# Kernel optimization log

Hardware: AMD Instinct MI355X
Metric: run time of the kernel (lower is better)

The kernel has to match this reference:

```python
import jax, jax.numpy as jnp
import numpy as np

NUM_HEADS = 8


def _attention(q, k, v, num_heads):
    # q,k,v: [L/S, N, E] seq-first (torch MHA convention)
    L, N, E = q.shape
    S = k.shape[0]
    hd = E // num_heads
    qh = q.reshape(L, N, num_heads, hd).transpose(1, 2, 0, 3)  # [N,H,L,hd]
    kh = k.reshape(S, N, num_heads, hd).transpose(1, 2, 0, 3)  # [N,H,S,hd]
    vh = v.reshape(S, N, num_heads, hd).transpose(1, 2, 0, 3)  # [N,H,S,hd]
    scale = 1.0 / np.sqrt(hd).astype(np.float32)
    scores = jnp.einsum('bhld,bhsd->bhls', qh * scale, kh)  # [N,H,L,S]
    probs = jax.nn.softmax(scores, axis=-1)
    out = jnp.einsum('bhls,bhsd->bhld', probs, vh)  # [N,H,L,hd]
    return out.transpose(2, 0, 1, 3).reshape(L, N, E)


def setup_inputs() -> dict:
    key = jax.random.key(0)
    ks = jax.random.split(key, 20)
    L, N, E = 1024, 8, 256
    s = 1.0 / np.sqrt(E)
    inp = {}
    names = ['query', 'key', 'value', 'query_teacher', 'key_teacher', 'value_teacher']
    for i, n in enumerate(names):
        inp[n] = jax.random.normal(ks[i], (L, N, E), dtype=jnp.float32)
    wnames = ['w_q', 'w_k', 'w_v', 'w_q_teacher', 'w_k_teacher', 'w_v_teacher', 'w_out', 'w_out_teacher']
    for i, n in enumerate(wnames):
        inp[n] = jax.random.normal(ks[6 + i], (E, E), dtype=jnp.float32) * s
    for n in ['b_q', 'b_k', 'b_v', 'b_q_teacher', 'b_k_teacher', 'b_v_teacher', 'b_out', 'b_out_teacher']:
        inp[n] = jnp.zeros((E,), dtype=jnp.float32)
    return inp


def reference(query, key, value, query_teacher, key_teacher, value_teacher,
              w_q, w_k, w_v, b_q, b_k, b_v,
              w_q_teacher, w_k_teacher, w_v_teacher, b_q_teacher, b_k_teacher, b_v_teacher,
              w_out, b_out, w_out_teacher, b_out_teacher):
    # Six separate in-projections (student + teacher), torch linear: x @ W.T + b
    Q = query @ w_q.T + b_q
    K = key @ w_k.T + b_k
    V = value @ w_v.T + b_v
    Qt = query_teacher @ w_q_teacher.T + b_q_teacher
    Kt = key_teacher @ w_k_teacher.T + b_k_teacher
    Vt = value_teacher @ w_v_teacher.T + b_v_teacher
    # Two attention streams
    out_s = _attention(Q, K, V, NUM_HEADS)
    out_t = _attention(Qt, Kt, Vt, NUM_HEADS)
    # Separate out-projections
    out_s = out_s @ w_out.T + b_out
    out_t = out_t @ w_out_teacher.T + b_out_teacher
    return out_s, out_t
```

## Files before the change

kernel.cpp:

```cpp
#include <hip/hip_runtime.h>

typedef __attribute__((ext_vector_type(4))) float f32x4;
typedef __attribute__((ext_vector_type(16))) float f32x16;
typedef __attribute__((ext_vector_type(8))) __bf16 bf16x8;
typedef __attribute__((ext_vector_type(4))) __bf16 bf16x4;

#define L_SEQ 1024
#define NB 8
#define EMB 256
#define NHEAD 8
#define HD 32
#define MROWS 8192
#define SZ_ELEM ((size_t)MROWS * EMB)

static __device__ __forceinline__ f32x4 mfma_bf16(bf16x8 a, bf16x8 b, f32x4 c) {
    return __builtin_amdgcn_mfma_f32_16x16x32_bf16(a, b, c, 0, 0, 0);
}
static __device__ __forceinline__ f32x16 mfma32(bf16x8 a, bf16x8 b, f32x16 c) {
    return __builtin_amdgcn_mfma_f32_32x32x16_bf16(a, b, c, 0, 0, 0);
}

static __device__ __forceinline__ unsigned pack2(float a, float b) {
    union { __bf16 h; unsigned short u; } lo, hi;
    lo.h = (__bf16)a; hi.h = (__bf16)b;
    return (unsigned)lo.u | ((unsigned)hi.u << 16);
}

static __device__ __forceinline__ void permswap(unsigned &a, unsigned &b) {
    asm("v_permlane32_swap_b32 %0, %1" : "+v"(a), "+v"(b));
}

struct GemmBatch {
    const void* X[6];
    const float* W[6];
    const float* Bv[6];
    void* O[6];
    float scale[6];
};

template<int XMODE, bool OUT_F32>
__global__ __launch_bounds__(256, 2)
void gemm_kernel(GemmBatch batch) {
    __shared__ __bf16 Xl[128][72];
    __shared__ __bf16 Wl[64][72];
    const int z = blockIdx.z;
    const int fid = blockIdx.x;
    const int swz = (fid & 7) * 32 + (fid >> 3);
    const int nblk = swz & 3, mblk = swz >> 2;
    const float* __restrict__ W = batch.W[z];
    const float* __restrict__ bias = batch.Bv[z];
    const float scale = batch.scale[z];
    const int tid = threadIdx.x;
    const int w = tid >> 6, lane = tid & 63;
    const int g = lane >> 4, li = lane & 15;
    const int wr = w >> 1, wc = w & 1;

    f32x4 acc[4][2];
#pragma unroll
    for (int i = 0; i < 4; ++i)
#pragma unroll
        for (int j = 0; j < 2; ++j) acc[i][j] = f32x4{0.f, 0.f, 0.f, 0.f};

    for (int kk = 0; kk < 4; ++kk) {
        __syncthreads();
        if (XMODE == 1) {
            const __bf16* Xb = (const __bf16*)batch.X[z];
#pragma unroll
            for (int p = 0; p < 4; ++p) {
                int idx = tid + p * 256;
                int row = idx >> 3, c8 = (idx & 7) * 8;
                bf16x8 xv = *(const bf16x8*)(Xb + (size_t)(mblk * 128 + row) * 256 + kk * 64 + c8);
                *(bf16x8*)&Xl[row][c8] = xv;
            }
        } else {
            const float* Xf = (const float*)batch.X[z];
#pragma unroll
            for (int p = 0; p < 8; ++p) {
                int idx = tid + p * 256;
                int row = idx >> 4, c4 = (idx & 15) * 4;
                f32x4 xv = *(const f32x4*)(Xf + (size_t)(mblk * 128 + row) * 256 + kk * 64 + c4);
                bf16x4 bv;
#pragma unroll
                for (int j = 0; j < 4; ++j) bv[j] = (__bf16)xv[j];
                *(bf16x4*)&Xl[row][c4] = bv;
            }
        }
#pragma unroll
        for (int p = 0; p < 4; ++p) {
            int idx = tid + p * 256;
            int row = idx >> 4, c4 = (idx & 15) * 4;
            f32x4 wv = *(const f32x4*)(W + (size_t)(nblk * 64 + row) * 256 + kk * 64 + c4);
            bf16x4 bv;
#pragma unroll
            for (int j = 0; j < 4; ++j) bv[j] = (__bf16)wv[j];
            *(bf16x4*)&Wl[row][c4] = bv;
        }
        __syncthreads();
#pragma unroll
        for (int ks = 0; ks < 2; ++ks) {
            bf16x8 a[4], b[2];
#pragma unroll
            for (int af = 0; af < 4; ++af)
                a[af] = *(const bf16x8*)&Xl[wr * 64 + af * 16 + li][ks * 32 + g * 8];
#pragma unroll
            for (int bi = 0; bi < 2; ++bi)
                b[bi] = *(const bf16x8*)&Wl[wc * 32 + bi * 16 + li][ks * 32 + g * 8];
#pragma unroll
            for (int af = 0; af < 4; ++af)
#pragma unroll
                for (int bi = 0; bi < 2; ++bi)
                    acc[af][bi] = mfma_bf16(a[af], b[bi], acc[af][bi]);
        }
    }
#pragma unroll
    for (int af = 0; af < 4; ++af)
#pragma unroll
        for (int bi = 0; bi < 2; ++bi)
#pragma unroll
            for (int r = 0; r < 4; ++r) {
                int mrow = mblk * 128 + wr * 64 + af * 16 + 4 * g + r;
                int ncol = nblk * 64 + wc * 32 + bi * 16 + li;
                float v = (acc[af][bi][r] + bias[ncol]) * scale;
                if (OUT_F32)
                    ((float*)batch.O[z])[(size_t)mrow * 256 + ncol] = v;
                else
                    ((__bf16*)batch.O[z])[(size_t)mrow * 256 + ncol] = (__bf16)v;
            }
}

struct AttnArgs {
    const __bf16* Q[2];
    const __bf16* K[2];
    const __bf16* V[2];
    __bf16* AO[2];
};

__global__ __launch_bounds__(256, 4)
void attn_kernel(AttnArgs args) {
    __shared__ __bf16 Kl[128][40];
    __shared__ __bf16 Vt[32][136];
    const int fid = blockIdx.x;
    const int swz = (fid & 7) * 128 + (fid >> 3);
    const int qb = swz & 7;
    const int nh = (swz >> 3) & 63;
    const int st = swz >> 9;
    const int n = nh >> 3, h = nh & 7;
    const __bf16* __restrict__ Q = args.Q[st];
    const __bf16* __restrict__ K = args.K[st];
    const __bf16* __restrict__ V = args.V[st];
    __bf16* __restrict__ AO = args.AO[st];
    const int tid = threadIdx.x;
    const int w = tid >> 6, lane = tid & 63;
    const int q32 = lane & 31, hi = lane >> 5;

    bf16x8 qf[2];
    {
        int qrow = qb * 128 + w * 32 + q32;
#pragma unroll
        for (int kb = 0; kb < 2; ++kb)
            qf[kb] = *(const bf16x8*)(Q + ((size_t)qrow * NB + n) * EMB + h * HD + kb * 16 + hi * 8);
    }

    bf16x8 ones;
#pragma unroll
    for (int j = 0; j < 8; ++j) ones[j] = (__bf16)1.0f;

    f32x16 accO, accL;
#pragma unroll
    for (int r = 0; r < 16; ++r) { accO[r] = 0.f; accL[r] = 0.f; }

    const int vsw_r = ((q32 >> 3) & 3) << 3;

    for (int t = 0; t < 8; ++t) {
        const int s0 = t * 128;
        __syncthreads();
#pragma unroll
        for (int p = 0; p < 2; ++p) {
            int idx = tid + p * 256;
            int row = idx >> 2, c8 = (idx & 3) * 8;
            size_t gaddr = ((size_t)(s0 + row) * NB + n) * EMB + h * HD + c8;
            *(bf16x8*)&Kl[row][c8] = *(const bf16x8*)(K + gaddr);
            bf16x8 vv = *(const bf16x8*)(V + gaddr);
#pragma unroll
            for (int j = 0; j < 8; ++j) {
                int d = c8 + j;
                Vt[d][row ^ (((d >> 3) & 3) << 3)] = vv[j];
            }
        }
        __syncthreads();

#pragma unroll
        for (int sb = 0; sb < 4; ++sb) {
            bf16x8 kf0 = *(const bf16x8*)&Kl[sb * 32 + q32][hi * 8];
            bf16x8 kf1 = *(const bf16x8*)&Kl[sb * 32 + q32][16 + hi * 8];
            f32x16 s;
#pragma unroll
            for (int r = 0; r < 16; ++r) s[r] = -12.0f;
            __builtin_amdgcn_s_setprio(1);
            s = mfma32(kf0, qf[0], s);
            s = mfma32(kf1, qf[1], s);
            __builtin_amdgcn_s_setprio(0);
            float p[16];
#pragma unroll
            for (int r = 0; r < 16; ++r) p[r] = __builtin_amdgcn_exp2f(s[r]);

            bf16x8 pa[2];
#pragma unroll
            for (int ks = 0; ks < 2; ++ks) {
                unsigned x0 = pack2(p[8 * ks + 0], p[8 * ks + 1]);
                unsigned x1 = pack2(p[8 * ks + 2], p[8 * ks + 3]);
                unsigned x2 = pack2(p[8 * ks + 4], p[8 * ks + 5]);
                unsigned x3 = pack2(p[8 * ks + 6], p[8 * ks + 7]);
                permswap(x0, x2);
                permswap(x1, x3);
                union { unsigned u[4]; bf16x8 v; } cvt;
                cvt.u[0] = x0; cvt.u[1] = x1; cvt.u[2] = x2; cvt.u[3] = x3;
                pa[ks] = cvt.v;
            }
            bf16x8 vf0 = *(const bf16x8*)&Vt[q32][(sb * 32 + hi * 8) ^ vsw_r];
            bf16x8 vf1 = *(const bf16x8*)&Vt[q32][(sb * 32 + 16 + hi * 8) ^ vsw_r];
            __builtin_amdgcn_s_setprio(1);
            accO = mfma32(pa[0], vf0, accO);
            accL = mfma32(pa[0], ones, accL);
            accO = mfma32(pa[1], vf1, accO);
            accL = mfma32(pa[1], ones, accL);
            __builtin_amdgcn_s_setprio(0);
        }
    }

#pragma unroll
    for (int r = 0; r < 16; ++r) {
        int crow = (r & 3) + 8 * (r >> 2) + 4 * hi;
        int row = qb * 128 + w * 32 + crow;
        AO[((size_t)row * NB + n) * EMB + h * HD + q32] = (__bf16)(accO[r] / accL[r]);
    }
}

extern "C" void kernel_launch(void* const* d_in, const int* in_sizes, int n_in,
                              void* d_out, int out_size, void* d_ws, size_t ws_size,
                              hipStream_t stream) {
    const size_t SZ = SZ_ELEM;
    __bf16* wsb = (__bf16*)d_ws;
    __bf16* arr[8];
    for (int i = 0; i < 8; ++i) arr[i] = wsb + (size_t)i * SZ;

    const float qscale = 0.25504310349362475f;

    GemmBatch pb{};
    for (int s = 0; s < 6; ++s) {
        pb.X[s] = d_in[s];
        pb.W[s] = (const float*)d_in[6 + s];
        pb.Bv[s] = (const float*)d_in[14 + s];
        pb.O[s] = arr[s];
        pb.scale[s] = (s == 0 || s == 3) ? qscale : 1.0f;
    }
    hipLaunchKernelGGL((gemm_kernel<0, false>), dim3(256, 1, 6), dim3(256), 0, stream, pb);

    AttnArgs aa{};
    aa.Q[0] = arr[0]; aa.K[0] = arr[1]; aa.V[0] = arr[2]; aa.AO[0] = arr[6];
    aa.Q[1] = arr[3]; aa.K[1] = arr[4]; aa.V[1] = arr[5]; aa.AO[1] = arr[7];
    hipLaunchKernelGGL(attn_kernel, dim3(1024), dim3(256), 0, stream, aa);

    GemmBatch ob{};
    for (int s = 0; s < 2; ++s) {
        ob.X[s] = arr[6 + s];
        ob.W[s] = (const float*)d_in[12 + s];
        ob.Bv[s] = (const float*)d_in[20 + s];
        ob.O[s] = (float*)d_out + (size_t)s * SZ;
        ob.scale[s] = 1.0f;
    }
    hipLaunchKernelGGL((gemm_kernel<1, true>), dim3(256, 1, 2), dim3(256), 0, stream, ob);
}
```

Before: 73.81 us.

## Double-buffer K/V shared tiles with register prefetch in attention loop

Attention now prefetches the next 128-row K/V tile into registers at the start of each iteration and writes it into a second LDS buffer after the compute phase. The goal is to hide global-load latency behind the QK/PV MFMA work. In exchange it doubles the LDS footprint and adds prefetch registers, which can lower occupancy. The score accumulator initialisation is also hoisted into a constant vector.

```diff
diff --git a/kernel.cpp b/kernel.cpp
--- a/kernel.cpp
+++ b/kernel.cpp
@@ -137,8 +137,8 @@
 
 __global__ __launch_bounds__(256, 4)
 void attn_kernel(AttnArgs args) {
-    __shared__ __bf16 Kl[128][40];
-    __shared__ __bf16 Vt[32][136];
+    __shared__ __bf16 Kl[2][128][40];
+    __shared__ __bf16 Vt[2][32][136];
     const int fid = blockIdx.x;
     const int swz = (fid & 7) * 128 + (fid >> 3);
     const int qb = swz & 7;
@@ -164,6 +164,9 @@
     bf16x8 ones;
 #pragma unroll
     for (int j = 0; j < 8; ++j) ones[j] = (__bf16)1.0f;
+    f32x16 minit;
+#pragma unroll
+    for (int r = 0; r < 16; ++r) minit[r] = -12.0f;
 
     f32x16 accO, accL;
 #pragma unroll
@@ -171,33 +174,41 @@
 
     const int vsw_r = ((q32 >> 3) & 3) << 3;
 
+    const int srow0 = tid >> 2, c8s = (tid & 3) * 8;
+    const int srow1 = srow0 + 64;
+
+    bf16x8 kreg[2], vreg[2];
+    {
+        size_t g0 = ((size_t)srow0 * NB + n) * EMB + h * HD + c8s;
+        size_t g1 = ((size_t)srow1 * NB + n) * EMB + h * HD + c8s;
+        kreg[0] = *(const bf16x8*)(K + g0); vreg[0] = *(const bf16x8*)(V + g0);
+        kreg[1] = *(const bf16x8*)(K + g1); vreg[1] = *(const bf16x8*)(V + g1);
+        *(bf16x8*)&Kl[0][srow0][c8s] = kreg[0];
+        *(bf16x8*)&Kl[0][srow1][c8s] = kreg[1];
+#pragma unroll
+        for (int j = 0; j < 8; ++j) {
+            int d = c8s + j, sw = ((d >> 3) & 3) << 3;
+            Vt[0][d][srow0 ^ sw] = vreg[0][j];
+            Vt[0][d][srow1 ^ sw] = vreg[1][j];
+        }
+    }
+    __syncthreads();
+
     for (int t = 0; t < 8; ++t) {
-        const int s0 = t * 128;
-        __syncthreads();
-#pragma unroll
-        for (int p = 0; p < 2; ++p) {
-            int idx = tid + p * 256;
-            int row = idx >> 2, c8 = (idx & 3) * 8;
-            size_t gaddr = ((size_t)(s0 + row) * NB + n) * EMB + h * HD + c8;
-            *(bf16x8*)&Kl[row][c8] = *(const bf16x8*)(K + gaddr);
-            bf16x8 vv = *(const bf16x8*)(V + gaddr);
-#pragma unroll
-            for (int j = 0; j < 8; ++j) {
-                int d = c8 + j;
-                Vt[d][row ^ (((d >> 3) & 3) << 3)] = vv[j];
-            }
-        }
-        __syncthreads();
+        const int buf = t & 1;
+        if (t < 7) {
+            size_t g0 = ((size_t)((t + 1) * 128 + srow0) * NB + n) * EMB + h * HD + c8s;
+            size_t g1 = ((size_t)((t + 1) * 128 + srow1) * NB + n) * EMB + h * HD + c8s;
+            kreg[0] = *(const bf16x8*)(K + g0); vreg[0] = *(const bf16x8*)(V + g0);
+            kreg[1] = *(const bf16x8*)(K + g1); vreg[1] = *(const bf16x8*)(V + g1);
+        }
 
 #pragma unroll
         for (int sb = 0; sb < 4; ++sb) {
-            bf16x8 kf0 = *(const bf16x8*)&Kl[sb * 32 + q32][hi * 8];
-            bf16x8 kf1 = *(const bf16x8*)&Kl[sb * 32 + q32][16 + hi * 8];
-            f32x16 s;
-#pragma unroll
-            for (int r = 0; r < 16; ++r) s[r] = -12.0f;
+            bf16x8 kf0 = *(const bf16x8*)&Kl[buf][sb * 32 + q32][hi * 8];
+            bf16x8 kf1 = *(const bf16x8*)&Kl[buf][sb * 32 + q32][16 + hi * 8];
             __builtin_amdgcn_s_setprio(1);
-            s = mfma32(kf0, qf[0], s);
+            f32x16 s = mfma32(kf0, qf[0], minit);
             s = mfma32(kf1, qf[1], s);
             __builtin_amdgcn_s_setprio(0);
             float p[16];
@@ -217,14 +228,28 @@
                 cvt.u[0] = x0; cvt.u[1] = x1; cvt.u[2] = x2; cvt.u[3] = x3;
                 pa[ks] = cvt.v;
             }
-            bf16x8 vf0 = *(const bf16x8*)&Vt[q32][(sb * 32 + hi * 8) ^ vsw_r];
-            bf16x8 vf1 = *(const bf16x8*)&Vt[q32][(sb * 32 + 16 + hi * 8) ^ vsw_r];
+            bf16x8 vf0 = *(const bf16x8*)&Vt[buf][q32][(sb * 32 + hi * 8) ^ vsw_r];
+            bf16x8 vf1 = *(const bf16x8*)&Vt[buf][q32][(sb * 32 + 16 + hi * 8) ^ vsw_r];
             __builtin_amdgcn_s_setprio(1);
             accO = mfma32(pa[0], vf0, accO);
             accL = mfma32(pa[0], ones, accL);
             accO = mfma32(pa[1], vf1, accO);
             accL = mfma32(pa[1], ones, accL);
             __builtin_amdgcn_s_setprio(0);
+        }
+
+        __syncthreads();
+        if (t < 7) {
+            const int nbuf = buf ^ 1;
+            *(bf16x8*)&Kl[nbuf][srow0][c8s] = kreg[0];
+            *(bf16x8*)&Kl[nbuf][srow1][c8s] = kreg[1];
+#pragma unroll
+            for (int j = 0; j < 8; ++j) {
+                int d = c8s + j, sw = ((d >> 3) & 3) << 3;
+                Vt[nbuf][d][srow0 ^ sw] = vreg[0][j];
+                Vt[nbuf][d][srow1 ^ sw] = vreg[1][j];
+            }
+            __syncthreads();
         }
     }
 
```

Result: no change. 74.23 us (+0.6%).
